# Optimization experiments

Measured on AMD Instinct MI355X. Metric: run time of the kernel, lower is better.

The kernel has to match this reference:

```python
import jax, jax.numpy as jnp
import numpy as np

N = 30000      # nodes
E = 480000     # edges (before self loops)
DIN = 128      # dim_in
DH = 32        # dim_h (per-head out channels)
H1 = 8         # gat1 heads
H2 = 2         # gat2 heads
G = 64         # num graphs in batch
DOUT = 10      # dim_out
NEG_SLOPE = 0.2


def _glorot(key, shape):
    fan_in = shape[0]
    return jax.random.normal(key, shape, dtype=jnp.float32) / np.sqrt(fan_in)


def setup_inputs() -> dict:
    key = jax.random.key(0)
    ks = jax.random.split(key, 16)
    x = jax.random.normal(ks[0], (N, DIN), dtype=jnp.float32)
    edge_index = jax.random.randint(ks[1], (2, E), 0, N, dtype=jnp.int32)
    batch = jnp.sort(jax.random.randint(ks[2], (N,), 0, G, dtype=jnp.int32))
    # GATv2Conv layer 1: lin_l, lin_r (dim_in -> H1*DH), att (H1, DH), bias (H1*DH)
    W1l = _glorot(ks[3], (DIN, H1 * DH))
    W1r = _glorot(ks[4], (DIN, H1 * DH))
    a1 = _glorot(ks[5], (DH, H1)).T  # [H1, DH]
    b1 = jnp.zeros((H1 * DH,), dtype=jnp.float32)
    # GATv2Conv layer 2: (H1*DH -> H2*DH)
    W2l = _glorot(ks[6], (H1 * DH, H2 * DH))
    W2r = _glorot(ks[7], (H1 * DH, H2 * DH))
    a2 = _glorot(ks[8], (DH, H2)).T  # [H2, DH]
    b2 = jnp.zeros((H2 * DH,), dtype=jnp.float32)
    # MLP head: fc1(2*DH -> DH), fc2(DH -> DH//2), fc(DH//2 -> DOUT); stored [in,out]
    fc1_w = _glorot(ks[9], (2 * DH, DH)); fc1_b = jnp.zeros((DH,), jnp.float32)
    fc2_w = _glorot(ks[10], (DH, DH // 2)); fc2_b = jnp.zeros((DH // 2,), jnp.float32)
    fc_w = _glorot(ks[11], (DH // 2, DOUT)); fc_b = jnp.zeros((DOUT,), jnp.float32)
    return {"x": x, "edge_index": edge_index, "batch": batch,
            "W1l": W1l, "W1r": W1r, "a1": a1, "b1": b1,
            "W2l": W2l, "W2r": W2r, "a2": a2, "b2": b2,
            "fc1_w": fc1_w, "fc1_b": fc1_b, "fc2_w": fc2_w, "fc2_b": fc2_b,
            "fc_w": fc_w, "fc_b": fc_b}


def gatv2_conv(x, edge_index, Wl, Wr, att, bias, heads, dh, n):
    """PyG GATv2Conv: concat=True, add_self_loops=True, negative_slope=0.2."""
    src, dst = edge_index[0], edge_index[1]
    loop = jnp.arange(n, dtype=src.dtype)        # self loops (PyG default)
    src = jnp.concatenate([src, loop])
    dst = jnp.concatenate([dst, loop])
    xl = (x @ Wl).reshape(n, heads, dh)          # source transform
    xr = (x @ Wr).reshape(n, heads, dh)          # destination transform
    xj = xl[src]                                  # [Etot, H, dh] message features
    s = jax.nn.leaky_relu(xj + xr[dst], NEG_SLOPE)
    e = jnp.einsum('ehd,hd->eh', s, att)          # per-edge per-head score
    # segment softmax over incoming edges of each destination node
    m = jax.ops.segment_max(e, dst, num_segments=n)
    p = jnp.exp(e - m[dst])
    z = jax.ops.segment_sum(p, dst, num_segments=n)
    alpha = p / z[dst]                            # [Etot, H]
    out = jax.ops.segment_sum(xj * alpha[..., None], dst, num_segments=n)
    return out.reshape(n, heads * dh) + bias


def reference(x, edge_index, batch, W1l, W1r, a1, b1, W2l, W2r, a2, b2,
              fc1_w, fc1_b, fc2_w, fc2_b, fc_w, fc_b):
    h = gatv2_conv(x, edge_index, W1l, W1r, a1, b1, H1, DH, N)
    h = jax.nn.elu(h)
    h = gatv2_conv(h, edge_index, W2l, W2r, a2, b2, H2, DH, N)  # [N, 2*DH]
    # global_mean_pool
    sums = jax.ops.segment_sum(h, batch, num_segments=G)
    cnt = jax.ops.segment_sum(jnp.ones((N,), h.dtype), batch, num_segments=G)
    hg = sums / jnp.maximum(cnt, 1.0)[:, None]    # [G, 2*DH]
    x1 = jax.nn.relu(hg @ fc1_w + fc1_b)
    # dropout p=0.2 is identity in eval mode
    x2 = jax.nn.relu(x1 @ fc2_w + fc2_b)
    c = x2 @ fc_w + fc_b
    return (c, x2)
```

## Files before the change

### kernel.cpp

```cpp
#include <hip/hip_runtime.h>
#include <math.h>

#define DIN 128
#define DH  32
#define H1  8
#define H2  2
#define GNUM 64
#define DOUT 10
#define NEG_SLOPE 0.2f
#define SCAN_B 512

typedef __attribute__((ext_vector_type(8))) short sv8;
typedef __attribute__((ext_vector_type(4))) short sv4;
typedef __attribute__((ext_vector_type(4))) float fv4;

static __device__ __forceinline__ unsigned short f2bf(float f) {
    unsigned int u = __float_as_uint(f);
    unsigned int r = (u + 0x7fffu + ((u >> 16) & 1u)) >> 16;
    return (unsigned short)r;
}
static __device__ __forceinline__ float bf2f(unsigned short h) {
    return __uint_as_float(((unsigned int)h) << 16);
}

__global__ void k_deg(const int* __restrict__ dst, int* __restrict__ deg, int E, int n) {
    int i = blockIdx.x * blockDim.x + threadIdx.x;
    if (i < E) {
        atomicAdd(&deg[dst[i]], 1);
    } else if (i < E + n) {
        atomicAdd(&deg[i - E], 1);
    }
}

__global__ __launch_bounds__(SCAN_B)
void k_scan_partial(const int* __restrict__ deg, int* __restrict__ bsum, int n) {
    int i = blockIdx.x * SCAN_B + threadIdx.x;
    int v = (i < n) ? deg[i] : 0;
    #pragma unroll
    for (int m = 32; m >= 1; m >>= 1) v += __shfl_xor(v, m);
    __shared__ int red[SCAN_B / 64];
    if ((threadIdx.x & 63) == 0) red[threadIdx.x >> 6] = v;
    __syncthreads();
    if (threadIdx.x == 0) {
        int s = 0;
        #pragma unroll
        for (int k = 0; k < SCAN_B / 64; ++k) s += red[k];
        bsum[blockIdx.x] = s;
    }
}

__global__ void k_scan_bsum(int* __restrict__ bsum, int nb) {
    if (threadIdx.x == 0 && blockIdx.x == 0) {
        int run = 0;
        for (int k = 0; k < nb; ++k) { int t = bsum[k]; bsum[k] = run; run += t; }
        bsum[nb] = run;
    }
}

__global__ __launch_bounds__(SCAN_B)
void k_scan_apply(int* __restrict__ deg, int* __restrict__ cursor,
                  const int* __restrict__ bsum, int n, int nb) {
    __shared__ int buf[SCAN_B];
    int t = threadIdx.x, b = blockIdx.x;
    int i = b * SCAN_B + t;
    int v = (i < n) ? deg[i] : 0;
    buf[t] = v;
    __syncthreads();
    for (int o = 1; o < SCAN_B; o <<= 1) {
        int a = (t >= o) ? buf[t - o] : 0;
        __syncthreads();
        buf[t] += a;
        __syncthreads();
    }
    int excl = buf[t] - v + bsum[b];
    if (i < n) { deg[i] = excl; cursor[i] = excl; }
    if (b == 0 && t == 0) deg[n] = bsum[nb];
}

__global__ void k_scatter(const int* __restrict__ src, const int* __restrict__ dst,
                          int* __restrict__ cursor, int* __restrict__ csr_src, int E, int n) {
    int i = blockIdx.x * blockDim.x + threadIdx.x;
    if (i < E) {
        int d = dst[i];
        int pos = atomicAdd(&cursor[d], 1);
        csr_src[pos] = src[i];
    } else if (i < E + n) {
        int v = i - E;
        int pos = atomicAdd(&cursor[v], 1);
        csr_src[pos] = v;
    }
}

__global__ void k_prep_bt(const float* __restrict__ Wl, const float* __restrict__ Wr,
                          short* __restrict__ Bth, short* __restrict__ Btl,
                          int K, int Nh) {
    int id = blockIdx.x * blockDim.x + threadIdx.x;
    int tot = 2 * Nh * K;
    if (id >= tot) return;
    int n = id / K, k = id - n * K;
    float v = (n < Nh) ? Wl[(size_t)k * Nh + n] : Wr[(size_t)k * Nh + (n - Nh)];
    unsigned short h = f2bf(v);
    Bth[id] = (short)h;
    Btl[id] = (short)f2bf(v - bf2f(h));
}

__global__ __launch_bounds__(256)
void k_gemm_mfma(const float* __restrict__ A, const short* __restrict__ Bth,
                 const short* __restrict__ Btl,
                 unsigned short* __restrict__ Cl, float* __restrict__ Cr,
                 int M, int K, int Ntot, int NL) {
    __shared__ union {
        struct { short hi[128 * 40]; short lo[128 * 40]; } a;
        float c[64 * 132];
    } sm;
    const int tid = threadIdx.x;
    const int lane = tid & 63;
    const int wid = tid >> 6;
    const int wm = wid & 1, wn = wid >> 1;
    const int m0 = blockIdx.x * 128;
    const int n0 = blockIdx.y * 128;
    const int l15 = lane & 15, q = lane >> 4;

    fv4 acc[4][4] = {};

    for (int kk = 0; kk < K; kk += 32) {
        __syncthreads();
        #pragma unroll
        for (int i = 0; i < 4; ++i) {
            int idx = tid + i * 256;
            int row = idx >> 3;
            int qq  = idx & 7;
            int mg  = m0 + row;
            float4 v = make_float4(0.f, 0.f, 0.f, 0.f);
            if (mg < M) v = *(const float4*)(A + (size_t)mg * K + kk + qq * 4);
            unsigned short hx = f2bf(v.x), hy = f2bf(v.y), hz = f2bf(v.z), hw = f2bf(v.w);
            sv4 hi = { (short)hx, (short)hy, (short)hz, (short)hw };
            sv4 lo = { (short)f2bf(v.x - bf2f(hx)), (short)f2bf(v.y - bf2f(hy)),
                       (short)f2bf(v.z - bf2f(hz)), (short)f2bf(v.w - bf2f(hw)) };
            *(sv4*)&sm.a.hi[row * 40 + qq * 4] = hi;
            *(sv4*)&sm.a.lo[row * 40 + qq * 4] = lo;
        }
        __syncthreads();

        sv8 bh[4], bl[4];
        #pragma unroll
        for (int fn = 0; fn < 4; ++fn) {
            int ng = n0 + wn * 64 + fn * 16 + l15;
            bh[fn] = *(const sv8*)(Bth + (size_t)ng * K + kk + q * 8);
            bl[fn] = *(const sv8*)(Btl + (size_t)ng * K + kk + q * 8);
        }
        #pragma unroll
        for (int fm = 0; fm < 4; ++fm) {
            int rl = wm * 64 + fm * 16 + l15;
            sv8 ah = *(const sv8*)&sm.a.hi[rl * 40 + q * 8];
            sv8 al = *(const sv8*)&sm.a.lo[rl * 40 + q * 8];
            #pragma unroll
            for (int fn = 0; fn < 4; ++fn) {
                acc[fm][fn] = __builtin_amdgcn_mfma_f32_16x16x32_bf16(ah, bh[fn], acc[fm][fn], 0, 0, 0);
                acc[fm][fn] = __builtin_amdgcn_mfma_f32_16x16x32_bf16(ah, bl[fn], acc[fm][fn], 0, 0, 0);
                acc[fm][fn] = __builtin_amdgcn_mfma_f32_16x16x32_bf16(al, bh[fn], acc[fm][fn], 0, 0, 0);
            }
        }
    }

    const int NR = Ntot - NL;
    #pragma unroll
    for (int s = 0; s < 2; ++s) {
        __syncthreads();
        if (wm == s) {
            #pragma unroll
            for (int fm = 0; fm < 4; ++fm)
                #pragma unroll
                for (int fn = 0; fn < 4; ++fn)
                    #pragma unroll
                    for (int r = 0; r < 4; ++r)
                        sm.c[(fm * 16 + q * 4 + r) * 132 + wn * 64 + fn * 16 + l15] = acc[fm][fn][r];
        }
        __syncthreads();
        #pragma unroll
        for (int i = 0; i < 2; ++i) {
            int lr = (tid >> 3) + i * 32;
            int grow = m0 + s * 64 + lr;
            if (grow < M) {
                #pragma unroll
                for (int k4 = 0; k4 < 4; ++k4) {
                    int jj = (tid & 7) + k4 * 8;
                    float4 vv = *(float4*)&sm.c[lr * 132 + jj * 4];
                    int gcol = n0 + jj * 4;
                    if (gcol < NL) {
                        ushort4 uu;
                        uu.x = f2bf(vv.x); uu.y = f2bf(vv.y);
                        uu.z = f2bf(vv.z); uu.w = f2bf(vv.w);
                        *(ushort4*)(Cl + (size_t)grow * NL + gcol) = uu;
                    } else {
                        *(float4*)(Cr + (size_t)grow * NR + (gcol - NL)) = vv;
                    }
                }
            }
        }
    }
}

static __device__ __forceinline__ void edge_acc(const float4 xl, const float4 xr,
                                                const float4 av, float& z, float4& acc) {
    float tx = xl.x + xr.x, ty = xl.y + xr.y, tz = xl.z + xr.z, tw = xl.w + xr.w;
    float lx = fmaxf(tx, 0.f) + NEG_SLOPE * fminf(tx, 0.f);
    float ly = fmaxf(ty, 0.f) + NEG_SLOPE * fminf(ty, 0.f);
    float lz = fmaxf(tz, 0.f) + NEG_SLOPE * fminf(tz, 0.f);
    float lw = fmaxf(tw, 0.f) + NEG_SLOPE * fminf(tw, 0.f);
    float s = lx * av.x + ly * av.y + lz * av.z + lw * av.w;
    s += __shfl_xor(s, 1);
    s += __shfl_xor(s, 2);
    s += __shfl_xor(s, 4);
    float w = __expf(s);
    z += w;
    acc.x = fmaf(w, xl.x, acc.x);
    acc.y = fmaf(w, xl.y, acc.y);
    acc.z = fmaf(w, xl.z, acc.z);
    acc.w = fmaf(w, xl.w, acc.w);
}

static __device__ __forceinline__ float4 bfx4(const ushort4 u) {
    float4 f;
    f.x = bf2f(u.x); f.y = bf2f(u.y); f.z = bf2f(u.z); f.w = bf2f(u.w);
    return f;
}

__global__ __launch_bounds__(256)
void k_edge1(const unsigned short* __restrict__ XLB, const float* __restrict__ XR,
             const int* __restrict__ offs, const int* __restrict__ csr,
             const float* __restrict__ att, const float* __restrict__ bias,
             float* __restrict__ out, int n) {
    const int lane = threadIdx.x & 63;
    const int wid  = threadIdx.x >> 6;
    const int v = blockIdx.x * 4 + wid;
    if (v >= n) return;
    const float4 xr = *(const float4*)(XR + (size_t)v * 256 + lane * 4);
    const float4 av = *(const float4*)(att + lane * 4);
    const float4 bv = *(const float4*)(bias + lane * 4);
    float z = 0.f;
    float4 acc = make_float4(0.f, 0.f, 0.f, 0.f);
    const int e0 = offs[v], e1 = offs[v + 1];
    int j = e0;
    for (; j + 2 <= e1; j += 2) {
        int s0 = csr[j], s1 = csr[j + 1];
        ushort4 u0 = *(const ushort4*)(XLB + (size_t)s0 * 256 + lane * 4);
        ushort4 u1 = *(const ushort4*)(XLB + (size_t)s1 * 256 + lane * 4);
        float4 x0 = bfx4(u0);
        float4 x1 = bfx4(u1);
        edge_acc(x0, xr, av, z, acc);
        edge_acc(x1, xr, av, z, acc);
    }
    if (j < e1) {
        int s0 = csr[j];
        ushort4 u0 = *(const ushort4*)(XLB + (size_t)s0 * 256 + lane * 4);
        edge_acc(bfx4(u0), xr, av, z, acc);
    }
    const float rz = 1.f / z;
    float4 o;
    o.x = fmaf(acc.x, rz, bv.x);
    o.y = fmaf(acc.y, rz, bv.y);
    o.z = fmaf(acc.z, rz, bv.z);
    o.w = fmaf(acc.w, rz, bv.w);
    o.x = (o.x > 0.f) ? o.x : (__expf(o.x) - 1.f);
    o.y = (o.y > 0.f) ? o.y : (__expf(o.y) - 1.f);
    o.z = (o.z > 0.f) ? o.z : (__expf(o.z) - 1.f);
    o.w = (o.w > 0.f) ? o.w : (__expf(o.w) - 1.f);
    *(float4*)(out + (size_t)v * 256 + lane * 4) = o;
}

__global__ __launch_bounds__(256)
void k_edge2(const unsigned short* __restrict__ XLB, const float* __restrict__ XR,
             const int* __restrict__ offs, const int* __restrict__ csr,
             const float* __restrict__ att, const float* __restrict__ bias,
             float* __restrict__ out, int n) {
    const int lane = threadIdx.x & 63;
    const int wid  = threadIdx.x >> 6;
    const int v = blockIdx.x * 4 + wid;
    if (v >= n) return;
    const int grp = lane >> 4, li = lane & 15;
    const float4 xr = *(const float4*)(XR + (size_t)v * 64 + li * 4);
    const float4 av = *(const float4*)(att + li * 4);
    float z = 0.f;
    float4 acc = make_float4(0.f, 0.f, 0.f, 0.f);
    const int e0 = offs[v], e1 = offs[v + 1];
    for (int j0 = e0; j0 < e1; j0 += 4) {
        const int j = j0 + grp;
        const bool valid = (j < e1);
        const int src = valid ? csr[j] : v;
        ushort4 u = *(const ushort4*)(XLB + (size_t)src * 64 + li * 4);
        float4 xl = bfx4(u);
        float tx = xl.x + xr.x, ty = xl.y + xr.y, tz = xl.z + xr.z, tw = xl.w + xr.w;
        float lx = fmaxf(tx, 0.f) + NEG_SLOPE * fminf(tx, 0.f);
        float ly = fmaxf(ty, 0.f) + NEG_SLOPE * fminf(ty, 0.f);
        float lz = fmaxf(tz, 0.f) + NEG_SLOPE * fminf(tz, 0.f);
        float lw = fmaxf(tw, 0.f) + NEG_SLOPE * fminf(tw, 0.f);
        float s = lx * av.x + ly * av.y + lz * av.z + lw * av.w;
        s += __shfl_xor(s, 1);
        s += __shfl_xor(s, 2);
        s += __shfl_xor(s, 4);
        float w = valid ? __expf(s) : 0.f;
        z += w;
        acc.x = fmaf(w, xl.x, acc.x);
        acc.y = fmaf(w, xl.y, acc.y);
        acc.z = fmaf(w, xl.z, acc.z);
        acc.w = fmaf(w, xl.w, acc.w);
    }
    z += __shfl_xor(z, 16); z += __shfl_xor(z, 32);
    acc.x += __shfl_xor(acc.x, 16); acc.x += __shfl_xor(acc.x, 32);
    acc.y += __shfl_xor(acc.y, 16); acc.y += __shfl_xor(acc.y, 32);
    acc.z += __shfl_xor(acc.z, 16); acc.z += __shfl_xor(acc.z, 32);
    acc.w += __shfl_xor(acc.w, 16); acc.w += __shfl_xor(acc.w, 32);
    if (grp == 0) {
        const float4 bv = *(const float4*)(bias + li * 4);
        const float rz = 1.f / z;
        float4 o;
        o.x = fmaf(acc.x, rz, bv.x);
        o.y = fmaf(acc.y, rz, bv.y);
        o.z = fmaf(acc.z, rz, bv.z);
        o.w = fmaf(acc.w, rz, bv.w);
        *(float4*)(out + (size_t)v * 64 + li * 4) = o;
    }
}

__global__ __launch_bounds__(256)
void k_pool(const float* __restrict__ out2, const int* __restrict__ batch,
            float* __restrict__ hg, int n) {
    const int g = blockIdx.x;
    const int lane = threadIdx.x & 63;
    const int w = threadIdx.x >> 6;
    int lo = 0, hi = n;
    while (lo < hi) { int mid = (lo + hi) >> 1; if (batch[mid] < g) lo = mid + 1; else hi = mid; }
    const int start = lo;
    hi = n;
    while (lo < hi) { int mid = (lo + hi) >> 1; if (batch[mid] < g + 1) lo = mid + 1; else hi = mid; }
    const int end = lo;

    float s = 0.f;
    for (int v = start + w; v < end; v += 4)
        s += out2[(size_t)v * 64 + lane];
    __shared__ float red[4][64];
    red[w][lane] = s;
    __syncthreads();
    if (w == 0) {
        float tot = red[0][lane] + red[1][lane] + red[2][lane] + red[3][lane];
        float cnt = fmaxf((float)(end - start), 1.0f);
        hg[g * 64 + lane] = tot / cnt;
    }
}

__global__ __launch_bounds__(64)
void k_mlp(const float* __restrict__ hgbuf,
           const float* __restrict__ fc1w, const float* __restrict__ fc1b,
           const float* __restrict__ fc2w, const float* __restrict__ fc2b,
           const float* __restrict__ fcw,  const float* __restrict__ fcb,
           float* __restrict__ outc, float* __restrict__ outx2) {
    const int g = blockIdx.x;
    const int t = threadIdx.x;
    __shared__ float hg_s[64];
    __shared__ float x1_s[32];
    __shared__ float x2_s[16];
    hg_s[t] = hgbuf[g * 64 + t];
    __syncthreads();
    if (t < 32) {
        float s = fc1b[t];
        #pragma unroll
        for (int k = 0; k < 64; ++k) s = fmaf(hg_s[k], fc1w[k * 32 + t], s);
        x1_s[t] = fmaxf(s, 0.f);
    }
    __syncthreads();
    if (t < 16) {
        float s = fc2b[t];
        #pragma unroll
        for (int k = 0; k < 32; ++k) s = fmaf(x1_s[k], fc2w[k * 16 + t], s);
        x2_s[t] = fmaxf(s, 0.f);
    }
    __syncthreads();
    if (t < DOUT) {
        float s = fcb[t];
        #pragma unroll
        for (int k = 0; k < 16; ++k) s = fmaf(x2_s[k], fcw[k * 10 + t], s);
        outc[g * DOUT + t] = s;
    }
    if (t < 16) outx2[g * 16 + t] = x2_s[t];
}

extern "C" void kernel_launch(void* const* d_in, const int* in_sizes, int n_in,
                              void* d_out, int out_size, void* d_ws, size_t ws_size,
                              hipStream_t stream) {
    const float* x    = (const float*)d_in[0];
    const int*   ei   = (const int*)d_in[1];
    const int*   batch= (const int*)d_in[2];
    const float* W1l  = (const float*)d_in[3];
    const float* W1r  = (const float*)d_in[4];
    const float* a1   = (const float*)d_in[5];
    const float* b1   = (const float*)d_in[6];
    const float* W2l  = (const float*)d_in[7];
    const float* W2r  = (const float*)d_in[8];
    const float* a2   = (const float*)d_in[9];
    const float* b2   = (const float*)d_in[10];
    const float* fc1w = (const float*)d_in[11];
    const float* fc1b = (const float*)d_in[12];
    const float* fc2w = (const float*)d_in[13];
    const float* fc2b = (const float*)d_in[14];
    const float* fcw  = (const float*)d_in[15];
    const float* fcb  = (const float*)d_in[16];

    const int N = in_sizes[2];
    const int E = in_sizes[1] / 2;
    const int ET = E + N;
    const int* esrc = ei;
    const int* edst = ei + E;
    const int NB = (N + SCAN_B - 1) / SCAN_B;

    char* ws = (char*)d_ws;
    size_t off = 0;
    unsigned short* xl1b = (unsigned short*)(ws + off);  off += (size_t)N * 256 * 2;
    float* xr1  = (float*)(ws + off);            off += (size_t)N * 256 * 4;
    float* h1   = (float*)(ws + off);            off += (size_t)N * 256 * 4;
    int*   deg   = (int*)(ws + off);             off += ((size_t)(N + 1) * 4 + 255) & ~255ull;
    int*   cursor= (int*)(ws + off);             off += ((size_t)N * 4 + 255) & ~255ull;
    int*   csr   = (int*)(ws + off);             off += ((size_t)ET * 4 + 255) & ~255ull;
    int*   bsum  = (int*)(ws + off);             off += ((size_t)(NB + 1) * 4 + 255) & ~255ull;
    float* hgbuf = (float*)(ws + off);           off += (size_t)GNUM * 64 * 4;
    short* B1th  = (short*)(ws + off);           off += (size_t)512 * 128 * 2;
    short* B1tl  = (short*)(ws + off);           off += (size_t)512 * 128 * 2;
    short* B2th  = (short*)(ws + off);           off += (size_t)128 * 256 * 2;
    short* B2tl  = (short*)(ws + off);           off += (size_t)128 * 256 * 2;
    unsigned short* xl2b = xl1b;
    float* xr2  = xr1;
    float* out2 = xr1 + (size_t)N * 64;
    (void)ws_size; (void)n_in; (void)out_size;

    float* outc  = (float*)d_out;
    float* outx2 = (float*)d_out + GNUM * DOUT;

    hipMemsetAsync(deg, 0, (size_t)(N + 1) * 4, stream);

    int tb = 256;
    int gb = (ET + tb - 1) / tb;
    k_deg<<<gb, tb, 0, stream>>>(edst, deg, E, N);
    k_scan_partial<<<NB, SCAN_B, 0, stream>>>(deg, bsum, N);
    k_scan_bsum<<<1, 64, 0, stream>>>(bsum, NB);
    k_scan_apply<<<NB, SCAN_B, 0, stream>>>(deg, cursor, bsum, N, NB);
    k_scatter<<<gb, tb, 0, stream>>>(esrc, edst, cursor, csr, E, N);

    k_prep_bt<<<(512 * 128 + 255) / 256, 256, 0, stream>>>(W1l, W1r, B1th, B1tl, DIN, 256);
    k_prep_bt<<<(128 * 256 + 255) / 256, 256, 0, stream>>>(W2l, W2r, B2th, B2tl, 256, 64);

    dim3 g1((N + 127) / 128, 4);
    k_gemm_mfma<<<g1, 256, 0, stream>>>(x, B1th, B1tl, xl1b, xr1, N, DIN, 512, 256);

    k_edge1<<<(N + 3) / 4, 256, 0, stream>>>(xl1b, xr1, deg, csr, a1, b1, h1, N);

    dim3 g2((N + 127) / 128, 1);
    k_gemm_mfma<<<g2, 256, 0, stream>>>(h1, B2th, B2tl, xl2b, xr2, N, 256, 128, 64);

    k_edge2<<<(N + 3) / 4, 256, 0, stream>>>(xl2b, xr2, deg, csr, a2, b2, out2, N);

    k_pool<<<GNUM, 256, 0, stream>>>(out2, batch, hgbuf, N);
    k_mlp<<<GNUM, 64, 0, stream>>>(hgbuf, fc1w, fc1b, fc2w, fc2b, fcw, fcb, outc, outx2);
}
```

Measured before the change: 338.1 us.

## Store layer-1 output as bf16, fuse small kernels, unroll edge gather

Layer-1 activations h1 are now written as bf16, and a new bf16-input MFMA GEMM for layer 2 uses only the hi part of A, which halves the h1 traffic and drops the A split. The block-sum scan is folded into k_scan_apply, the two weight-prep launches are merged, and pooling is fused with the MLP to cut launch count. The edge1 gather loop is unrolled to 4 edges for more memory-level parallelism. Dropping the A low part lowers layer-2 input precision to bf16. The in-kernel scan assumes at most 64 scan blocks.

```diff
diff --git a/kernel.cpp b/kernel.cpp
--- a/kernel.cpp
+++ b/kernel.cpp
@@ -49,19 +49,24 @@
     }
 }
 
-__global__ void k_scan_bsum(int* __restrict__ bsum, int nb) {
-    if (threadIdx.x == 0 && blockIdx.x == 0) {
-        int run = 0;
-        for (int k = 0; k < nb; ++k) { int t = bsum[k]; bsum[k] = run; run += t; }
-        bsum[nb] = run;
-    }
-}
-
 __global__ __launch_bounds__(SCAN_B)
 void k_scan_apply(int* __restrict__ deg, int* __restrict__ cursor,
                   const int* __restrict__ bsum, int n, int nb) {
     __shared__ int buf[SCAN_B];
-    int t = threadIdx.x, b = blockIdx.x;
+    __shared__ int pfx_s, tot_s;
+    const int t = threadIdx.x, b = blockIdx.x;
+    if (t < 64) {
+        int v = (t < nb) ? bsum[t] : 0;
+        int incl = v;
+        #pragma unroll
+        for (int o = 1; o < 64; o <<= 1) {
+            int w = __shfl_up(incl, o);
+            if (t >= o) incl += w;
+        }
+        int pfx = (b == 0) ? 0 : __shfl(incl, b - 1);
+        int tot = __shfl(incl, nb - 1);
+        if (t == 0) { pfx_s = pfx; tot_s = tot; }
+    }
     int i = b * SCAN_B + t;
     int v = (i < n) ? deg[i] : 0;
     buf[t] = v;
@@ -72,9 +77,9 @@
         buf[t] += a;
         __syncthreads();
     }
-    int excl = buf[t] - v + bsum[b];
+    int excl = buf[t] - v + pfx_s;
     if (i < n) { deg[i] = excl; cursor[i] = excl; }
-    if (b == 0 && t == 0) deg[n] = bsum[nb];
+    if (b == 0 && t == 0) deg[n] = tot_s;
 }
 
 __global__ void k_scatter(const int* __restrict__ src, const int* __restrict__ dst,
@@ -91,17 +96,27 @@
     }
 }
 
-__global__ void k_prep_bt(const float* __restrict__ Wl, const float* __restrict__ Wr,
-                          short* __restrict__ Bth, short* __restrict__ Btl,
-                          int K, int Nh) {
+__global__ void k_prep(const float* __restrict__ W1l, const float* __restrict__ W1r,
+                       const float* __restrict__ W2l, const float* __restrict__ W2r,
+                       short* __restrict__ B1th, short* __restrict__ B1tl,
+                       short* __restrict__ B2th, short* __restrict__ B2tl) {
     int id = blockIdx.x * blockDim.x + threadIdx.x;
-    int tot = 2 * Nh * K;
-    if (id >= tot) return;
-    int n = id / K, k = id - n * K;
-    float v = (n < Nh) ? Wl[(size_t)k * Nh + n] : Wr[(size_t)k * Nh + (n - Nh)];
-    unsigned short h = f2bf(v);
-    Bth[id] = (short)h;
-    Btl[id] = (short)f2bf(v - bf2f(h));
+    const int T1 = 512 * 128;
+    const int T2 = 128 * 256;
+    if (id < T1) {
+        int n = id / 128, k = id - n * 128;
+        float v = (n < 256) ? W1l[(size_t)k * 256 + n] : W1r[(size_t)k * 256 + (n - 256)];
+        unsigned short h = f2bf(v);
+        B1th[id] = (short)h;
+        B1tl[id] = (short)f2bf(v - bf2f(h));
+    } else if (id < T1 + T2) {
+        int id2 = id - T1;
+        int n = id2 / 256, k = id2 - n * 256;
+        float v = (n < 64) ? W2l[(size_t)k * 64 + n] : W2r[(size_t)k * 64 + (n - 64)];
+        unsigned short h = f2bf(v);
+        B2th[id2] = (short)h;
+        B2tl[id2] = (short)f2bf(v - bf2f(h));
+    }
 }
 
 __global__ __launch_bounds__(256)
@@ -201,6 +216,96 @@
     }
 }
 
+__global__ __launch_bounds__(256)
+void k_gemm_mfma_bf(const unsigned short* __restrict__ A, const short* __restrict__ Bth,
+                    const short* __restrict__ Btl,
+                    unsigned short* __restrict__ Cl, float* __restrict__ Cr,
+                    int M, int K, int Ntot, int NL) {
+    __shared__ union {
+        short a[128 * 40];
+        float c[64 * 132];
+    } sm;
+    const int tid = threadIdx.x;
+    const int lane = tid & 63;
+    const int wid = tid >> 6;
+    const int wm = wid & 1, wn = wid >> 1;
+    const int m0 = blockIdx.x * 128;
+    const int n0 = blockIdx.y * 128;
+    const int l15 = lane & 15, q = lane >> 4;
+
+    fv4 acc[4][4] = {};
+
+    for (int kk = 0; kk < K; kk += 32) {
+        __syncthreads();
+        #pragma unroll
+        for (int i = 0; i < 2; ++i) {
+            int idx = tid + i * 256;
+            int row = idx >> 2;
+            int qq  = idx & 3;
+            int mg  = m0 + row;
+            sv8 v = { 0, 0, 0, 0, 0, 0, 0, 0 };
+            if (mg < M) v = *(const sv8*)(A + (size_t)mg * K + kk + qq * 8);
+            *(sv8*)&sm.a[row * 40 + qq * 8] = v;
+        }
+        __syncthreads();
+
+        sv8 bh[4], bl[4];
+        #pragma unroll
+        for (int fn = 0; fn < 4; ++fn) {
+            int ng = n0 + wn * 64 + fn * 16 + l15;
+            bh[fn] = *(const sv8*)(Bth + (size_t)ng * K + kk + q * 8);
+            bl[fn] = *(const sv8*)(Btl + (size_t)ng * K + kk + q * 8);
+        }
+        #pragma unroll
+        for (int fm = 0; fm < 4; ++fm) {
+            int rl = wm * 64 + fm * 16 + l15;
+            sv8 ah = *(const sv8*)&sm.a[rl * 40 + q * 8];
+            #pragma unroll
+            for (int fn = 0; fn < 4; ++fn) {
+                acc[fm][fn] = __builtin_amdgcn_mfma_f32_16x16x32_bf16(ah, bh[fn], acc[fm][fn], 0, 0, 0);
+                acc[fm][fn] = __builtin_amdgcn_mfma_f32_16x16x32_bf16(ah, bl[fn], acc[fm][fn], 0, 0, 0);
+            }
+        }
+    }
+
+    const int NR = Ntot - NL;
+    #pragma unroll
+    for (int s = 0; s < 2; ++s) {
+        __syncthreads();
+        if (wm == s) {
+            #pragma unroll
+            for (int fm = 0; fm < 4; ++fm)
+                #pragma unroll
+                for (int fn = 0; fn < 4; ++fn)
+                    #pragma unroll
+                    for (int r = 0; r < 4; ++r)
+                        sm.c[(fm * 16 + q * 4 + r) * 132 + wn * 64 + fn * 16 + l15] = acc[fm][fn][r];
+        }
+        __syncthreads();
+        #pragma unroll
+        for (int i = 0; i < 2; ++i) {
+            int lr = (tid >> 3) + i * 32;
+            int grow = m0 + s * 64 + lr;
+            if (grow < M) {
+                #pragma unroll
+                for (int k4 = 0; k4 < 4; ++k4) {
+                    int jj = (tid & 7) + k4 * 8;
+                    float4 vv = *(float4*)&sm.c[lr * 132 + jj * 4];
+                    int gcol = n0 + jj * 4;
+                    if (gcol < NL) {
+                        ushort4 uu;
+                        uu.x = f2bf(vv.x); uu.y = f2bf(vv.y);
+                        uu.z = f2bf(vv.z); uu.w = f2bf(vv.w);
+                        *(ushort4*)(Cl + (size_t)grow * NL + gcol) = uu;
+                    } else {
+                        *(float4*)(Cr + (size_t)grow * NR + (gcol - NL)) = vv;
+                    }
+                }
+            }
+        }
+    }
+}
+
 static __device__ __forceinline__ void edge_acc(const float4 xl, const float4 xr,
                                                 const float4 av, float& z, float4& acc) {
     float tx = xl.x + xr.x, ty = xl.y + xr.y, tz = xl.z + xr.z, tw = xl.w + xr.w;
@@ -230,7 +335,7 @@
 void k_edge1(const unsigned short* __restrict__ XLB, const float* __restrict__ XR,
              const int* __restrict__ offs, const int* __restrict__ csr,
              const float* __restrict__ att, const float* __restrict__ bias,
-             float* __restrict__ out, int n) {
+             unsigned short* __restrict__ out, int n) {
     const int lane = threadIdx.x & 63;
     const int wid  = threadIdx.x >> 6;
     const int v = blockIdx.x * 4 + wid;
@@ -242,16 +347,18 @@
     float4 acc = make_float4(0.f, 0.f, 0.f, 0.f);
     const int e0 = offs[v], e1 = offs[v + 1];
     int j = e0;
-    for (; j + 2 <= e1; j += 2) {
-        int s0 = csr[j], s1 = csr[j + 1];
+    for (; j + 4 <= e1; j += 4) {
+        int s0 = csr[j], s1 = csr[j + 1], s2 = csr[j + 2], s3 = csr[j + 3];
         ushort4 u0 = *(const ushort4*)(XLB + (size_t)s0 * 256 + lane * 4);
         ushort4 u1 = *(const ushort4*)(XLB + (size_t)s1 * 256 + lane * 4);
-        float4 x0 = bfx4(u0);
-        float4 x1 = bfx4(u1);
-        edge_acc(x0, xr, av, z, acc);
-        edge_acc(x1, xr, av, z, acc);
-    }
-    if (j < e1) {
+        ushort4 u2 = *(const ushort4*)(XLB + (size_t)s2 * 256 + lane * 4);
+        ushort4 u3 = *(const ushort4*)(XLB + (size_t)s3 * 256 + lane * 4);
+        edge_acc(bfx4(u0), xr, av, z, acc);
+        edge_acc(bfx4(u1), xr, av, z, acc);
+        edge_acc(bfx4(u2), xr, av, z, acc);
+        edge_acc(bfx4(u3), xr, av, z, acc);
+    }
+    for (; j < e1; ++j) {
         int s0 = csr[j];
         ushort4 u0 = *(const ushort4*)(XLB + (size_t)s0 * 256 + lane * 4);
         edge_acc(bfx4(u0), xr, av, z, acc);
@@ -266,7 +373,9 @@
     o.y = (o.y > 0.f) ? o.y : (__expf(o.y) - 1.f);
     o.z = (o.z > 0.f) ? o.z : (__expf(o.z) - 1.f);
     o.w = (o.w > 0.f) ? o.w : (__expf(o.w) - 1.f);
-    *(float4*)(out + (size_t)v * 256 + lane * 4) = o;
+    ushort4 hv;
+    hv.x = f2bf(o.x); hv.y = f2bf(o.y); hv.z = f2bf(o.z); hv.w = f2bf(o.w);
+    *(ushort4*)(out + (size_t)v * 256 + lane * 4) = hv;
 }
 
 __global__ __launch_bounds__(256)
@@ -324,11 +433,20 @@
 }
 
 __global__ __launch_bounds__(256)
-void k_pool(const float* __restrict__ out2, const int* __restrict__ batch,
-            float* __restrict__ hg, int n) {
+void k_pool_mlp(const float* __restrict__ out2, const int* __restrict__ batch,
+                const float* __restrict__ fc1w, const float* __restrict__ fc1b,
+                const float* __restrict__ fc2w, const float* __restrict__ fc2b,
+                const float* __restrict__ fcw,  const float* __restrict__ fcb,
+                float* __restrict__ outc, float* __restrict__ outx2, int n) {
     const int g = blockIdx.x;
-    const int lane = threadIdx.x & 63;
-    const int w = threadIdx.x >> 6;
+    const int t = threadIdx.x;
+    const int lane = t & 63;
+    const int w = t >> 6;
+    __shared__ float red[4][64];
+    __shared__ float hg_s[64];
+    __shared__ float x1_s[32];
+    __shared__ float x2_s[16];
+
     int lo = 0, hi = n;
     while (lo < hi) { int mid = (lo + hi) >> 1; if (batch[mid] < g) lo = mid + 1; else hi = mid; }
     const int start = lo;
@@ -339,48 +457,33 @@
     float s = 0.f;
     for (int v = start + w; v < end; v += 4)
         s += out2[(size_t)v * 64 + lane];
-    __shared__ float red[4][64];
     red[w][lane] = s;
     __syncthreads();
     if (w == 0) {
         float tot = red[0][lane] + red[1][lane] + red[2][lane] + red[3][lane];
         float cnt = fmaxf((float)(end - start), 1.0f);
-        hg[g * 64 + lane] = tot / cnt;
-    }
-}
-
-__global__ __launch_bounds__(64)
-void k_mlp(const float* __restrict__ hgbuf,
-           const float* __restrict__ fc1w, const float* __restrict__ fc1b,
-           const float* __restrict__ fc2w, const float* __restrict__ fc2b,
-           const float* __restrict__ fcw,  const float* __restrict__ fcb,
-           float* __restrict__ outc, float* __restrict__ outx2) {
-    const int g = blockIdx.x;
-    const int t = threadIdx.x;
-    __shared__ float hg_s[64];
-    __shared__ float x1_s[32];
-    __shared__ float x2_s[16];
-    hg_s[t] = hgbuf[g * 64 + t];
+        hg_s[lane] = tot / cnt;
+    }
     __syncthreads();
     if (t < 32) {
-        float s = fc1b[t];
-        #pragma unroll
-        for (int k = 0; k < 64; ++k) s = fmaf(hg_s[k], fc1w[k * 32 + t], s);
-        x1_s[t] = fmaxf(s, 0.f);
+        float a = fc1b[t];
+        #pragma unroll
+        for (int k = 0; k < 64; ++k) a = fmaf(hg_s[k], fc1w[k * 32 + t], a);
+        x1_s[t] = fmaxf(a, 0.f);
     }
     __syncthreads();
     if (t < 16) {
-        float s = fc2b[t];
-        #pragma unroll
-        for (int k = 0; k < 32; ++k) s = fmaf(x1_s[k], fc2w[k * 16 + t], s);
-        x2_s[t] = fmaxf(s, 0.f);
+        float a = fc2b[t];
+        #pragma unroll
+        for (int k = 0; k < 32; ++k) a = fmaf(x1_s[k], fc2w[k * 16 + t], a);
+        x2_s[t] = fmaxf(a, 0.f);
     }
     __syncthreads();
     if (t < DOUT) {
-        float s = fcb[t];
-        #pragma unroll
-        for (int k = 0; k < 16; ++k) s = fmaf(x2_s[k], fcw[k * 10 + t], s);
-        outc[g * DOUT + t] = s;
+        float a = fcb[t];
+        #pragma unroll
+        for (int k = 0; k < 16; ++k) a = fmaf(x2_s[k], fcw[k * 10 + t], a);
+        outc[g * DOUT + t] = a;
     }
     if (t < 16) outx2[g * 16 + t] = x2_s[t];
 }
@@ -417,12 +520,11 @@
     size_t off = 0;
     unsigned short* xl1b = (unsigned short*)(ws + off);  off += (size_t)N * 256 * 2;
     float* xr1  = (float*)(ws + off);            off += (size_t)N * 256 * 4;
-    float* h1   = (float*)(ws + off);            off += (size_t)N * 256 * 4;
+    unsigned short* h1b = (unsigned short*)(ws + off);   off += (size_t)N * 256 * 2;
     int*   deg   = (int*)(ws + off);             off += ((size_t)(N + 1) * 4 + 255) & ~255ull;
     int*   cursor= (int*)(ws + off);             off += ((size_t)N * 4 + 255) & ~255ull;
     int*   csr   = (int*)(ws + off);             off += ((size_t)ET * 4 + 255) & ~255ull;
     int*   bsum  = (int*)(ws + off);             off += ((size_t)(NB + 1) * 4 + 255) & ~255ull;
-    float* hgbuf = (float*)(ws + off);           off += (size_t)GNUM * 64 * 4;
     short* B1th  = (short*)(ws + off);           off += (size_t)512 * 128 * 2;
     short* B1tl  = (short*)(ws + off);           off += (size_t)512 * 128 * 2;
     short* B2th  = (short*)(ws + off);           off += (size_t)128 * 256 * 2;
@@ -441,23 +543,22 @@
     int gb = (ET + tb - 1) / tb;
     k_deg<<<gb, tb, 0, stream>>>(edst, deg, E, N);
     k_scan_partial<<<NB, SCAN_B, 0, stream>>>(deg, bsum, N);
-    k_scan_bsum<<<1, 64, 0, stream>>>(bsum, NB);
     k_scan_apply<<<NB, SCAN_B, 0, stream>>>(deg, cursor, bsum, N, NB);
     k_scatter<<<gb, tb, 0, stream>>>(esrc, edst, cursor, csr, E, N);
 
-    k_prep_bt<<<(512 * 128 + 255) / 256, 256, 0, stream>>>(W1l, W1r, B1th, B1tl, DIN, 256);
-    k_prep_bt<<<(128 * 256 + 255) / 256, 256, 0, stream>>>(W2l, W2r, B2th, B2tl, 256, 64);
+    k_prep<<<(512 * 128 + 128 * 256 + 255) / 256, 256, 0, stream>>>(
+        W1l, W1r, W2l, W2r, B1th, B1tl, B2th, B2tl);
 
     dim3 g1((N + 127) / 128, 4);
     k_gemm_mfma<<<g1, 256, 0, stream>>>(x, B1th, B1tl, xl1b, xr1, N, DIN, 512, 256);
 
-    k_edge1<<<(N + 3) / 4, 256, 0, stream>>>(xl1b, xr1, deg, csr, a1, b1, h1, N);
+    k_edge1<<<(N + 3) / 4, 256, 0, stream>>>(xl1b, xr1, deg, csr, a1, b1, h1b, N);
 
     dim3 g2((N + 127) / 128, 1);
-    k_gemm_mfma<<<g2, 256, 0, stream>>>(h1, B2th, B2tl, xl2b, xr2, N, 256, 128, 64);
+    k_gemm_mfma_bf<<<g2, 256, 0, stream>>>(h1b, B2th, B2tl, xl2b, xr2, N, 256, 128, 64);
 
     k_edge2<<<(N + 3) / 4, 256, 0, stream>>>(xl2b, xr2, deg, csr, a2, b2, out2, N);
 
-    k_pool<<<GNUM, 256, 0, stream>>>(out2, batch, hgbuf, N);
-    k_mlp<<<GNUM, 64, 0, stream>>>(hgbuf, fc1w, fc1b, fc2w, fc2b, fcw, fcb, outc, outx2);
-}
+    k_pool_mlp<<<GNUM, 256, 0, stream>>>(out2, batch, fc1w, fc1b, fc2w, fc2b,
+                                         fcw, fcb, outc, outx2, N);
+}
```

Result: faster. 317.5 us (-6.1%).
